# Kernel tuning notes

Measured on AMD Instinct MI355X. Metric: run time of the kernel, lower is better.

The kernel has to match this reference:

```python
import jax, jax.numpy as jnp
import numpy as np
import math

D_MODEL = 1024
NUM_HEADS = 16
HEAD_DIM = D_MODEL // NUM_HEADS
GAMMA = 1.0
B, T = 2, 2048
PHI_F = 8


def setup_inputs() -> dict:
    key = jax.random.key(0)
    ks = jax.random.split(key, 16)
    s = 0.02
    return {
        "query": jax.random.normal(ks[0], (B, T, D_MODEL), jnp.float32),
        "key": jax.random.normal(ks[1], (B, T, D_MODEL), jnp.float32),
        "value": jax.random.normal(ks[2], (B, T, D_MODEL), jnp.float32),
        "phi": jax.random.uniform(ks[3], (B, T, PHI_F), jnp.float32),
        "logvar": jax.random.normal(ks[4], (B, T, PHI_F), jnp.float32),
        "Wq": jax.random.normal(ks[5], (D_MODEL, D_MODEL), jnp.float32) * s,
        "bq": jnp.zeros((D_MODEL,), jnp.float32),
        "Wk": jax.random.normal(ks[6], (D_MODEL, D_MODEL), jnp.float32) * s,
        "bk": jnp.zeros((D_MODEL,), jnp.float32),
        "Wv": jax.random.normal(ks[7], (D_MODEL, D_MODEL), jnp.float32) * s,
        "bv": jnp.zeros((D_MODEL,), jnp.float32),
        "Wo": jax.random.normal(ks[8], (D_MODEL, D_MODEL), jnp.float32) * s,
        "bo": jnp.zeros((D_MODEL,), jnp.float32),
        "w_sigma": jnp.float32(1.0),
        "w_phi": jnp.float32(1.0),
    }


def reference(query, key, value, phi, logvar, Wq, bq, Wk, bk, Wv, bv, Wo, bo, w_sigma, w_phi):
    Bsz, Tq, _ = query.shape
    # projections (torch Linear: x @ W.T + b), split into heads -> (B, H, T, hd)
    def proj(x, W, b):
        return (x @ W.T + b).reshape(Bsz, Tq, NUM_HEADS, HEAD_DIM).transpose(0, 2, 1, 3)
    q = proj(query, Wq, bq)
    k = proj(key, Wk, bk)
    v = proj(value, Wv, bv)
    # raw scores (B, H, Tq, Tk)
    scores = jnp.einsum("bhqd,bhkd->bhqk", q, k) / math.sqrt(HEAD_DIM)
    # per-query token scalar biases: mean over feature dim -> (B, 1, T, 1)
    lv = logvar.mean(axis=-1)[:, None, :, None]
    ph = phi.mean(axis=-1)[:, None, :, None]
    scores = scores - w_sigma * lv
    scores = (scores - w_phi * (1.0 - ph)) / jnp.maximum(ph ** GAMMA, 1e-6)
    attn = jax.nn.softmax(scores, axis=-1)
    out = jnp.einsum("bhqk,bhkd->bhqd", attn, v)
    out = out.transpose(0, 2, 1, 3).reshape(Bsz, Tq, D_MODEL)
    return out @ Wo.T + bo
```

## Files before the change

### kernel.cpp

```cpp
#include <hip/hip_runtime.h>


typedef __bf16 bf16x8 __attribute__((ext_vector_type(8)));
typedef float f32x4 __attribute__((ext_vector_type(4)));
typedef unsigned short u16;
typedef unsigned int u32;
typedef u16 u16x8 __attribute__((ext_vector_type(8)));

#define GLD_TO_LDS(g, l) __builtin_amdgcn_global_load_lds( \
    (const __attribute__((address_space(1))) void*)(g),    \
    (__attribute__((address_space(3))) void*)(l), 16, 0, 0)

__device__ __forceinline__ u16 f2b(float f) {
  u32 u = __builtin_bit_cast(u32, f);
  u += 0x7fffu + ((u >> 16) & 1u);
  return (u16)(u >> 16);
}

__global__ __launch_bounds__(256) void prep_kernel(
    const float* __restrict__ query, const float* __restrict__ key,
    const float* __restrict__ value, const float* __restrict__ Wq,
    const float* __restrict__ Wk, const float* __restrict__ Wv,
    const float* __restrict__ Wo, const float* __restrict__ phi,
    u16* __restrict__ Xq, u16* __restrict__ Xk, u16* __restrict__ Xv,
    u16* __restrict__ Wqb, u16* __restrict__ Wkb, u16* __restrict__ Wvb,
    u16* __restrict__ Wob, float* __restrict__ rscale)
{
  const long gid = (long)blockIdx.x * 256 + threadIdx.x;
  const long e = gid * 4;
  const float* src; u16* dst; long off;
  if (e < 4194304L)       { src = query; dst = Xq;  off = e; }
  else if (e < 8388608L)  { src = key;   dst = Xk;  off = e - 4194304L; }
  else if (e < 12582912L) { src = value; dst = Xv;  off = e - 8388608L; }
  else if (e < 13631488L) { src = Wq;    dst = Wqb; off = e - 12582912L; }
  else if (e < 14680064L) { src = Wk;    dst = Wkb; off = e - 13631488L; }
  else if (e < 15728640L) { src = Wv;    dst = Wvb; off = e - 14680064L; }
  else                    { src = Wo;    dst = Wob; off = e - 15728640L; }
  const float4 v = *(const float4*)(src + off);
  ushort4 o;
  o.x = f2b(v.x); o.y = f2b(v.y); o.z = f2b(v.z); o.w = f2b(v.w);
  *(ushort4*)(dst + off) = o;

  if (gid < 4096) {
    const float4 p0 = *(const float4*)(phi + gid * 8);
    const float4 p1 = *(const float4*)(phi + gid * 8 + 4);
    const float mean = (p0.x + p0.y + p0.z + p0.w + p1.x + p1.y + p1.z + p1.w) * 0.125f;
    rscale[gid] = 1.4426950408889634f / (8.0f * fmaxf(mean, 1e-6f));
  }
}

template<int MODE>
__device__ __forceinline__ void gemm_body(
    u16* As, u16* Bs,
    const u16* __restrict__ A, const u16* __restrict__ Bw,
    const float* __restrict__ bias, void* __restrict__ Cout)
{
  constexpr int K = 1024;
  const int t = threadIdx.x;
  const int lane = t & 63, w = t >> 6;
  const int g = lane >> 4, c = lane & 15;
  const int m0 = blockIdx.y * 128, n0 = blockIdx.x * 128;
  const int srow = t >> 2, skc = (t & 3) * 8;
  const u16* gA = A + (size_t)(m0 + srow) * K + skc;
  const u16* gB = Bw + (size_t)(n0 + srow) * K + skc;
  u16* ldsA = As + w * 512;
  u16* ldsB = Bs + w * 512;
  const int wm = (w >> 1) * 64, wn = (w & 1) * 64;

  f32x4 acc[4][4] = {};

  for (int k0 = 0; k0 < K; k0 += 32) {
    GLD_TO_LDS(gA + k0, ldsA);
    GLD_TO_LDS(gA + 64 * K + k0, ldsA + 2048);
    GLD_TO_LDS(gB + k0, ldsB);
    GLD_TO_LDS(gB + 64 * K + k0, ldsB + 2048);
    __syncthreads();
    bf16x8 af[4], bfr[4];
#pragma unroll
    for (int mi = 0; mi < 4; ++mi)
      af[mi] = *(const bf16x8*)(As + (wm + mi * 16 + c) * 32 + g * 8);
#pragma unroll
    for (int ni = 0; ni < 4; ++ni)
      bfr[ni] = *(const bf16x8*)(Bs + (wn + ni * 16 + c) * 32 + g * 8);
#pragma unroll
    for (int mi = 0; mi < 4; ++mi)
#pragma unroll
      for (int ni = 0; ni < 4; ++ni)
        acc[mi][ni] = __builtin_amdgcn_mfma_f32_16x16x32_bf16(
            af[mi], bfr[ni], acc[mi][ni], 0, 0, 0);
    __syncthreads();
  }

#pragma unroll
  for (int ni = 0; ni < 4; ++ni) {
    const int ncol = n0 + wn + ni * 16 + c;
    const float bv = bias[ncol];
#pragma unroll
    for (int mi = 0; mi < 4; ++mi) {
#pragma unroll
      for (int r = 0; r < 4; ++r) {
        const int mrow = m0 + wm + mi * 16 + g * 4 + r;
        const float val = acc[mi][ni][r] + bv;
        if (MODE == 0) {
          const int bb = mrow >> 11, tt = mrow & 2047;
          const int hh = ncol >> 6, dd = ncol & 63;
          ((u16*)Cout)[((((size_t)bb * 16 + hh) * 2048 + tt) << 6) + dd] = f2b(val);
        } else {
          ((float*)Cout)[(size_t)mrow * 1024 + ncol] = val;
        }
      }
    }
  }
}

__global__ __launch_bounds__(256) void gemm_qkv_kernel(
    const u16* __restrict__ Xq, const u16* __restrict__ Xk, const u16* __restrict__ Xv,
    const u16* __restrict__ Wqb, const u16* __restrict__ Wkb, const u16* __restrict__ Wvb,
    const float* __restrict__ bq, const float* __restrict__ bk, const float* __restrict__ bv,
    u16* __restrict__ Qh, u16* __restrict__ Kh, u16* __restrict__ Vh)
{
  __shared__ __align__(16) u16 As[4096], Bs[4096];
  const int z = blockIdx.z;
  const u16* A = (z == 0) ? Xq : (z == 1) ? Xk : Xv;
  const u16* W = (z == 0) ? Wqb : (z == 1) ? Wkb : Wvb;
  const float* bias = (z == 0) ? bq : (z == 1) ? bk : bv;
  u16* C = (z == 0) ? Qh : (z == 1) ? Kh : Vh;
  gemm_body<0>(As, Bs, A, W, bias, C);
}

__global__ __launch_bounds__(256) void gemm_o_kernel(
    const u16* __restrict__ Oh, const u16* __restrict__ Wob,
    const float* __restrict__ bo, float* __restrict__ out)
{
  __shared__ __align__(16) u16 As[4096], Bs[4096];
  gemm_body<1>(As, Bs, Oh, Wob, bo, out);
}

__global__ __launch_bounds__(256) void transpose_v_kernel(
    const u16* __restrict__ Vh, u16* __restrict__ Vt)
{
  __shared__ __align__(16) u16 tile[64][72];
  const int bh = blockIdx.y, t0 = blockIdx.x * 64;
  const int tid = threadIdx.x;
  const int r = tid >> 3, cc = (tid & 7) * 8;
  const u16* src = Vh + ((size_t)bh * 2048 + t0) * 64;
#pragma unroll
  for (int it = 0; it < 2; ++it)
    *(u16x8*)&tile[r + 32 * it][cc] = *(const u16x8*)(src + (size_t)(r + 32 * it) * 64 + cc);
  __syncthreads();
  u16* dst = Vt + (size_t)bh * 64 * 2048 + t0;
#pragma unroll
  for (int it = 0; it < 2; ++it) {
    const int d = r + 32 * it;
    u16x8 v;
#pragma unroll
    for (int j = 0; j < 8; ++j) v[j] = tile[cc + j][d];
    *(u16x8*)(dst + (size_t)d * 2048 + cc) = v;
  }
}

__global__ __launch_bounds__(256) void attn_kernel(
    const u16* __restrict__ Qh, const u16* __restrict__ Kh,
    const u16* __restrict__ Vt, const float* __restrict__ rscale,
    u16* __restrict__ Oh)
{
  __shared__ __align__(16) u16 Ks[2][4096];
  __shared__ __align__(16) u16 Vs[2][4096];
  __shared__ __align__(16) u16 Pl[4][1024];

  const u32 orig = blockIdx.y * 32 + blockIdx.x;
  const u32 newL = (orig & 7u) * 128u + (orig >> 3);
  const int qx = newL & 31, bh = newL >> 5;
  const int b = bh >> 4, h = bh & 15;

  const int t = threadIdx.x;
  const int w = t >> 6, lane = t & 63;
  const int g = lane >> 4, c = lane & 15;
  const int q0 = qx * 64 + w * 16;
  const int swz = (c & 7) << 4;

  const u16* Qb = Qh + (size_t)bh * (2048 * 64);
  const u16* Kb = Kh + (size_t)bh * (2048 * 64);
  const u16* Vb = Vt + (size_t)bh * (64 * 2048);

  const int sr = t >> 3;
  const int sx = ((t & 7) ^ (sr & 7)) * 8;

  const float rs = rscale[b * 2048 + q0 + c];
  bf16x8 qf0, qf1;
  {
    const u16x8 a0 = *(const u16x8*)(Qb + (size_t)(q0 + c) * 64 + g * 8);
    const u16x8 a1 = *(const u16x8*)(Qb + (size_t)(q0 + c) * 64 + 32 + g * 8);
    u16x8 o0, o1;
#pragma unroll
    for (int j = 0; j < 8; ++j) {
      o0[j] = f2b(__builtin_bit_cast(float, (u32)a0[j] << 16) * rs);
      o1[j] = f2b(__builtin_bit_cast(float, (u32)a1[j] << 16) * rs);
    }
    qf0 = __builtin_bit_cast(bf16x8, o0);
    qf1 = __builtin_bit_cast(bf16x8, o1);
  }

  float m[4], l[4];
#pragma unroll
  for (int r = 0; r < 4; ++r) { m[r] = -3.0e38f; l[r] = 0.0f; }
  f32x4 acc[4] = {};
  u16* const Pw = &Pl[w][0];

#define STAGE(buf_, kc_) do {                                         \
    const u16* kg0 = Kb + (size_t)((kc_) + sr) * 64 + sx;             \
    const u16* kg1 = Kb + (size_t)((kc_) + 32 + sr) * 64 + sx;        \
    const u16* vg0 = Vb + (size_t)sr * 2048 + (kc_) + sx;             \
    const u16* vg1 = Vb + (size_t)(32 + sr) * 2048 + (kc_) + sx;      \
    u16* kd = &Ks[buf_][w * 512];                                     \
    u16* vd = &Vs[buf_][w * 512];                                     \
    GLD_TO_LDS(kg0, kd);                                              \
    GLD_TO_LDS(kg1, kd + 2048);                                       \
    GLD_TO_LDS(vg0, vd);                                              \
    GLD_TO_LDS(vg1, vd + 2048);                                       \
  } while (0)

  STAGE(0, 0);

  for (int kc = 0; kc < 2048; kc += 64) {
    const int buf = (kc >> 6) & 1;
    if (kc + 64 < 2048) {
      STAGE(buf ^ 1, kc + 64);
      asm volatile("s_waitcnt vmcnt(4)" ::: "memory");
    } else {
      asm volatile("s_waitcnt vmcnt(0)" ::: "memory");
    }
    __builtin_amdgcn_s_barrier();

    const u16* Kt = &Ks[buf][0];
    const u16* Vq = &Vs[buf][0];

    f32x4 s[4];
#pragma unroll
    for (int j = 0; j < 4; ++j) {
      const int rk = j * 16 + c;
      const bf16x8 k0 = *(const bf16x8*)(Kt + rk * 64 + ((((g << 4)) ^ swz) >> 1));
      const bf16x8 k1 = *(const bf16x8*)(Kt + rk * 64 + (((64 | (g << 4)) ^ swz) >> 1));
      const f32x4 z = {};
      s[j] = __builtin_amdgcn_mfma_f32_16x16x32_bf16(qf0, k0, z, 0, 0, 0);
      s[j] = __builtin_amdgcn_mfma_f32_16x16x32_bf16(qf1, k1, s[j], 0, 0, 0);
    }

    bf16x8 vf[4][2];
#pragma unroll
    for (int dt = 0; dt < 4; ++dt) {
      const int rv = dt * 16 + c;
#pragma unroll
      for (int kk = 0; kk < 2; ++kk)
        vf[dt][kk] = *(const bf16x8*)(Vq + rv * 64 + ((((kk << 6) | (g << 4)) ^ swz) >> 1));
    }

    float tl[4];
    bool need = false;
#pragma unroll
    for (int r = 0; r < 4; ++r) {
      tl[r] = fmaxf(fmaxf(s[0][r], s[1][r]), fmaxf(s[2][r], s[3][r]));
      need |= (tl[r] > m[r] + 8.0f);
    }
    if (__any(need)) {
#pragma unroll
      for (int d = 1; d < 16; d <<= 1)
#pragma unroll
        for (int r = 0; r < 4; ++r)
          tl[r] = fmaxf(tl[r], __shfl_xor(tl[r], d));
#pragma unroll
      for (int r = 0; r < 4; ++r) {
        const float mn = fmaxf(m[r], tl[r]);
        const float corr = __builtin_amdgcn_exp2f(m[r] - mn);
        m[r] = mn;
        l[r] *= corr;
#pragma unroll
        for (int dt = 0; dt < 4; ++dt) acc[dt][r] *= corr;
      }
    }

#pragma unroll
    for (int j = 0; j < 4; ++j)
#pragma unroll
      for (int r = 0; r < 4; ++r) {
        const float p = __builtin_amdgcn_exp2f(s[j][r] - m[r]);
        l[r] += p;
        const int prow = g * 4 + r;
        Pw[prow * 64 + ((((j * 16 + c) * 2) ^ ((prow & 7) << 4)) >> 1)] = f2b(p);
      }
    const bf16x8 pA0 = *(const bf16x8*)(Pw + c * 64 + (((0 | (g << 4)) ^ swz) >> 1));
    const bf16x8 pA1 = *(const bf16x8*)(Pw + c * 64 + (((64 | (g << 4)) ^ swz) >> 1));
#pragma unroll
    for (int dt = 0; dt < 4; ++dt) {
      acc[dt] = __builtin_amdgcn_mfma_f32_16x16x32_bf16(pA0, vf[dt][0], acc[dt], 0, 0, 0);
      acc[dt] = __builtin_amdgcn_mfma_f32_16x16x32_bf16(pA1, vf[dt][1], acc[dt], 0, 0, 0);
    }

    __builtin_amdgcn_s_barrier();
  }
#undef STAGE

#pragma unroll
  for (int d = 1; d < 16; d <<= 1)
#pragma unroll
    for (int r = 0; r < 4; ++r)
      l[r] += __shfl_xor(l[r], d);

  float inv[4];
#pragma unroll
  for (int r = 0; r < 4; ++r) inv[r] = 1.0f / l[r];
#pragma unroll
  for (int dt = 0; dt < 4; ++dt)
#pragma unroll
    for (int r = 0; r < 4; ++r) {
      const int trow = q0 + g * 4 + r;
      const int dd = dt * 16 + c;
      Oh[(((size_t)b * 2048 + trow) * 16 + h) * 64 + dd] = f2b(acc[dt][r] * inv[r]);
    }
}

extern "C" void kernel_launch(void* const* d_in, const int* in_sizes, int n_in,
                              void* d_out, int out_size, void* d_ws, size_t ws_size,
                              hipStream_t stream) {
  const float* query = (const float*)d_in[0];
  const float* key_  = (const float*)d_in[1];
  const float* value = (const float*)d_in[2];
  const float* phi   = (const float*)d_in[3];
  const float* Wq = (const float*)d_in[5];
  const float* bq = (const float*)d_in[6];
  const float* Wk = (const float*)d_in[7];
  const float* bk = (const float*)d_in[8];
  const float* Wv = (const float*)d_in[9];
  const float* bv = (const float*)d_in[10];
  const float* Wo = (const float*)d_in[11];
  const float* bo = (const float*)d_in[12];

  char* ws = (char*)d_ws;
  const size_t MB = 1u << 20;
  u16* Xq  = (u16*)(ws);
  u16* Xk  = (u16*)(ws + 8 * MB);
  u16* Xv  = (u16*)(ws + 16 * MB);
  u16* Wqb = (u16*)(ws + 24 * MB);
  u16* Wkb = (u16*)(ws + 26 * MB);
  u16* Wvb = (u16*)(ws + 28 * MB);
  u16* Wob = (u16*)(ws + 30 * MB);
  u16* Qh  = (u16*)(ws + 32 * MB);
  u16* Kh  = (u16*)(ws + 40 * MB);
  u16* Vh  = (u16*)(ws + 48 * MB);
  float* rscale = (float*)(ws + 56 * MB);
  u16* Oh = Xq;
  u16* Vt = Xk;

  prep_kernel<<<16384, 256, 0, stream>>>(query, key_, value, Wq, Wk, Wv, Wo, phi,
                                         Xq, Xk, Xv, Wqb, Wkb, Wvb, Wob, rscale);
  gemm_qkv_kernel<<<dim3(8, 32, 3), 256, 0, stream>>>(Xq, Xk, Xv, Wqb, Wkb, Wvb,
                                                      bq, bk, bv, Qh, Kh, Vh);
  transpose_v_kernel<<<dim3(32, 32), 256, 0, stream>>>(Vh, Vt);
  attn_kernel<<<dim3(32, 32), 256, 0, stream>>>(Qh, Kh, Vt, rscale, Oh);
  gemm_o_kernel<<<dim3(8, 32), 256, 0, stream>>>(Oh, Wob, bo, (float*)d_out);
}
```

Baseline: 288.0 us.

## Transpose attention MFMAs to keep P in registers; double-buffer GEMMs with swizzled grid

The attention kernel now computes S^T (K as A operand, Q as B), so each lane holds a single query column. The probabilities can then be packed straight into bf16 MFMA operands with no LDS round-trip for P. The row max and sum collapse to one scalar per lane, cutting the shuffles, and V fragments are gathered with 4-element LDS reads. The projection GEMMs gain double-buffered LDS staging with vmcnt waits, plus a block-index remap intended to improve L2 reuse. The costs are doubled GEMM LDS use and more V-load instructions.

```diff
diff --git a/kernel.cpp b/kernel.cpp
--- a/kernel.cpp
+++ b/kernel.cpp
@@ -2,6 +2,7 @@
 
 
 typedef __bf16 bf16x8 __attribute__((ext_vector_type(8)));
+typedef __bf16 bf16x4 __attribute__((ext_vector_type(4)));
 typedef float f32x4 __attribute__((ext_vector_type(4)));
 typedef unsigned short u16;
 typedef unsigned int u32;
@@ -51,7 +52,7 @@
 
 template<int MODE>
 __device__ __forceinline__ void gemm_body(
-    u16* As, u16* Bs,
+    u16 (*As)[4096], u16 (*Bs)[4096], int m0, int n0,
     const u16* __restrict__ A, const u16* __restrict__ Bw,
     const float* __restrict__ bias, void* __restrict__ Cout)
 {
@@ -59,37 +60,46 @@
   const int t = threadIdx.x;
   const int lane = t & 63, w = t >> 6;
   const int g = lane >> 4, c = lane & 15;
-  const int m0 = blockIdx.y * 128, n0 = blockIdx.x * 128;
   const int srow = t >> 2, skc = (t & 3) * 8;
   const u16* gA = A + (size_t)(m0 + srow) * K + skc;
   const u16* gB = Bw + (size_t)(n0 + srow) * K + skc;
-  u16* ldsA = As + w * 512;
-  u16* ldsB = Bs + w * 512;
   const int wm = (w >> 1) * 64, wn = (w & 1) * 64;
 
   f32x4 acc[4][4] = {};
 
-  for (int k0 = 0; k0 < K; k0 += 32) {
-    GLD_TO_LDS(gA + k0, ldsA);
-    GLD_TO_LDS(gA + 64 * K + k0, ldsA + 2048);
-    GLD_TO_LDS(gB + k0, ldsB);
-    GLD_TO_LDS(gB + 64 * K + k0, ldsB + 2048);
-    __syncthreads();
+#define STG(b_, k0_) do {                              \
+    GLD_TO_LDS(gA + (k0_), &As[b_][w * 512]);          \
+    GLD_TO_LDS(gA + 64 * K + (k0_), &As[b_][w * 512 + 2048]); \
+    GLD_TO_LDS(gB + (k0_), &Bs[b_][w * 512]);          \
+    GLD_TO_LDS(gB + 64 * K + (k0_), &Bs[b_][w * 512 + 2048]); \
+  } while (0)
+
+  STG(0, 0);
+  for (int i = 0; i < 32; ++i) {
+    const int buf = i & 1;
+    if (i < 31) {
+      STG(buf ^ 1, (i + 1) * 32);
+      asm volatile("s_waitcnt vmcnt(4)" ::: "memory");
+    } else {
+      asm volatile("s_waitcnt vmcnt(0)" ::: "memory");
+    }
+    __builtin_amdgcn_s_barrier();
     bf16x8 af[4], bfr[4];
 #pragma unroll
     for (int mi = 0; mi < 4; ++mi)
-      af[mi] = *(const bf16x8*)(As + (wm + mi * 16 + c) * 32 + g * 8);
+      af[mi] = *(const bf16x8*)(&As[buf][0] + (wm + mi * 16 + c) * 32 + g * 8);
 #pragma unroll
     for (int ni = 0; ni < 4; ++ni)
-      bfr[ni] = *(const bf16x8*)(Bs + (wn + ni * 16 + c) * 32 + g * 8);
+      bfr[ni] = *(const bf16x8*)(&Bs[buf][0] + (wn + ni * 16 + c) * 32 + g * 8);
 #pragma unroll
     for (int mi = 0; mi < 4; ++mi)
 #pragma unroll
       for (int ni = 0; ni < 4; ++ni)
         acc[mi][ni] = __builtin_amdgcn_mfma_f32_16x16x32_bf16(
             af[mi], bfr[ni], acc[mi][ni], 0, 0, 0);
-    __syncthreads();
-  }
+    __builtin_amdgcn_s_barrier();
+  }
+#undef STG
 
 #pragma unroll
   for (int ni = 0; ni < 4; ++ni) {
@@ -119,21 +129,25 @@
     const float* __restrict__ bq, const float* __restrict__ bk, const float* __restrict__ bv,
     u16* __restrict__ Qh, u16* __restrict__ Kh, u16* __restrict__ Vh)
 {
-  __shared__ __align__(16) u16 As[4096], Bs[4096];
-  const int z = blockIdx.z;
-  const u16* A = (z == 0) ? Xq : (z == 1) ? Xk : Xv;
-  const u16* W = (z == 0) ? Wqb : (z == 1) ? Wkb : Wvb;
-  const float* bias = (z == 0) ? bq : (z == 1) ? bk : bv;
-  u16* C = (z == 0) ? Qh : (z == 1) ? Kh : Vh;
-  gemm_body<0>(As, Bs, A, W, bias, C);
+  __shared__ __align__(16) u16 As[2][4096], Bs[2][4096];
+  const u32 n = blockIdx.z * 256u + blockIdx.y * 8u + blockIdx.x;
+  const u32 nl = (n & 7u) * 96u + (n >> 3);
+  const int bx = nl & 7, by = (nl >> 3) & 31, bz = nl >> 8;
+  const u16* A = (bz == 0) ? Xq : (bz == 1) ? Xk : Xv;
+  const u16* W = (bz == 0) ? Wqb : (bz == 1) ? Wkb : Wvb;
+  const float* bias = (bz == 0) ? bq : (bz == 1) ? bk : bv;
+  u16* C = (bz == 0) ? Qh : (bz == 1) ? Kh : Vh;
+  gemm_body<0>(As, Bs, by * 128, bx * 128, A, W, bias, C);
 }
 
 __global__ __launch_bounds__(256) void gemm_o_kernel(
     const u16* __restrict__ Oh, const u16* __restrict__ Wob,
     const float* __restrict__ bo, float* __restrict__ out)
 {
-  __shared__ __align__(16) u16 As[4096], Bs[4096];
-  gemm_body<1>(As, Bs, Oh, Wob, bo, out);
+  __shared__ __align__(16) u16 As[2][4096], Bs[2][4096];
+  const u32 n = blockIdx.y * 8u + blockIdx.x;
+  const u32 nl = (n & 7u) * 32u + (n >> 3);
+  gemm_body<1>(As, Bs, (int)(nl >> 3) * 128, (int)(nl & 7) * 128, Oh, Wob, bo, out);
 }
 
 __global__ __launch_bounds__(256) void transpose_v_kernel(
@@ -166,7 +180,6 @@
 {
   __shared__ __align__(16) u16 Ks[2][4096];
   __shared__ __align__(16) u16 Vs[2][4096];
-  __shared__ __align__(16) u16 Pl[4][1024];
 
   const u32 orig = blockIdx.y * 32 + blockIdx.x;
   const u32 newL = (orig & 7u) * 128u + (orig >> 3);
@@ -201,11 +214,8 @@
     qf1 = __builtin_bit_cast(bf16x8, o1);
   }
 
-  float m[4], l[4];
-#pragma unroll
-  for (int r = 0; r < 4; ++r) { m[r] = -3.0e38f; l[r] = 0.0f; }
+  float m = -3.0e38f, l = 0.0f;
   f32x4 acc[4] = {};
-  u16* const Pw = &Pl[w][0];
 
 #define STAGE(buf_, kc_) do {                                         \
     const u16* kg0 = Kb + (size_t)((kc_) + sr) * 64 + sx;             \
@@ -242,80 +252,77 @@
       const bf16x8 k0 = *(const bf16x8*)(Kt + rk * 64 + ((((g << 4)) ^ swz) >> 1));
       const bf16x8 k1 = *(const bf16x8*)(Kt + rk * 64 + (((64 | (g << 4)) ^ swz) >> 1));
       const f32x4 z = {};
-      s[j] = __builtin_amdgcn_mfma_f32_16x16x32_bf16(qf0, k0, z, 0, 0, 0);
-      s[j] = __builtin_amdgcn_mfma_f32_16x16x32_bf16(qf1, k1, s[j], 0, 0, 0);
-    }
-
-    bf16x8 vf[4][2];
+      s[j] = __builtin_amdgcn_mfma_f32_16x16x32_bf16(k0, qf0, z, 0, 0, 0);
+      s[j] = __builtin_amdgcn_mfma_f32_16x16x32_bf16(k1, qf1, s[j], 0, 0, 0);
+    }
+
+    float tl = s[0][0];
+#pragma unroll
+    for (int j = 0; j < 4; ++j)
+#pragma unroll
+      for (int r = 0; r < 4; ++r) tl = fmaxf(tl, s[j][r]);
+    if (__any(tl > m + 8.0f)) {
+      tl = fmaxf(tl, __shfl_xor(tl, 16));
+      tl = fmaxf(tl, __shfl_xor(tl, 32));
+      const float mn = fmaxf(m, tl);
+      const float corr = __builtin_amdgcn_exp2f(m - mn);
+      m = mn;
+      l *= corr;
+#pragma unroll
+      for (int dt = 0; dt < 4; ++dt)
+#pragma unroll
+        for (int r = 0; r < 4; ++r) acc[dt][r] *= corr;
+    }
+
+    float p[4][4];
+#pragma unroll
+    for (int j = 0; j < 4; ++j)
+#pragma unroll
+      for (int r = 0; r < 4; ++r) {
+        p[j][r] = __builtin_amdgcn_exp2f(s[j][r] - m);
+        l += p[j][r];
+      }
+    bf16x8 pb0, pb1;
+#pragma unroll
+    for (int jj = 0; jj < 8; ++jj) {
+      pb0[jj] = (__bf16)p[jj >> 2][jj & 3];
+      pb1[jj] = (__bf16)p[2 + (jj >> 2)][jj & 3];
+    }
+
 #pragma unroll
     for (int dt = 0; dt < 4; ++dt) {
       const int rv = dt * 16 + c;
-#pragma unroll
-      for (int kk = 0; kk < 2; ++kk)
-        vf[dt][kk] = *(const bf16x8*)(Vq + rv * 64 + ((((kk << 6) | (g << 4)) ^ swz) >> 1));
-    }
-
-    float tl[4];
-    bool need = false;
+      const u16* vrow = Vq + rv * 64;
+      const int xr = (rv & 7) << 4;
+      bf16x8 va0, va1;
+      const bf16x4 a0 = *(const bf16x4*)(vrow + (((g * 8) ^ xr) >> 1));
+      const bf16x4 a1 = *(const bf16x4*)(vrow + (((32 + g * 8) ^ xr) >> 1));
+      const bf16x4 a2 = *(const bf16x4*)(vrow + (((64 + g * 8) ^ xr) >> 1));
+      const bf16x4 a3 = *(const bf16x4*)(vrow + (((96 + g * 8) ^ xr) >> 1));
+#pragma unroll
+      for (int j = 0; j < 4; ++j) {
+        va0[j] = a0[j]; va0[4 + j] = a1[j];
+        va1[j] = a2[j]; va1[4 + j] = a3[j];
+      }
+      acc[dt] = __builtin_amdgcn_mfma_f32_16x16x32_bf16(va0, pb0, acc[dt], 0, 0, 0);
+      acc[dt] = __builtin_amdgcn_mfma_f32_16x16x32_bf16(va1, pb1, acc[dt], 0, 0, 0);
+    }
+
+    __builtin_amdgcn_s_barrier();
+  }
+#undef STAGE
+
+  l += __shfl_xor(l, 16);
+  l += __shfl_xor(l, 32);
+  const float inv = 1.0f / l;
+
+#pragma unroll
+  for (int dt = 0; dt < 4; ++dt)
 #pragma unroll
     for (int r = 0; r < 4; ++r) {
-      tl[r] = fmaxf(fmaxf(s[0][r], s[1][r]), fmaxf(s[2][r], s[3][r]));
-      need |= (tl[r] > m[r] + 8.0f);
-    }
-    if (__any(need)) {
-#pragma unroll
-      for (int d = 1; d < 16; d <<= 1)
-#pragma unroll
-        for (int r = 0; r < 4; ++r)
-          tl[r] = fmaxf(tl[r], __shfl_xor(tl[r], d));
-#pragma unroll
-      for (int r = 0; r < 4; ++r) {
-        const float mn = fmaxf(m[r], tl[r]);
-        const float corr = __builtin_amdgcn_exp2f(m[r] - mn);
-        m[r] = mn;
-        l[r] *= corr;
-#pragma unroll
-        for (int dt = 0; dt < 4; ++dt) acc[dt][r] *= corr;
-      }
-    }
-
-#pragma unroll
-    for (int j = 0; j < 4; ++j)
-#pragma unroll
-      for (int r = 0; r < 4; ++r) {
-        const float p = __builtin_amdgcn_exp2f(s[j][r] - m[r]);
-        l[r] += p;
-        const int prow = g * 4 + r;
-        Pw[prow * 64 + ((((j * 16 + c) * 2) ^ ((prow & 7) << 4)) >> 1)] = f2b(p);
-      }
-    const bf16x8 pA0 = *(const bf16x8*)(Pw + c * 64 + (((0 | (g << 4)) ^ swz) >> 1));
-    const bf16x8 pA1 = *(const bf16x8*)(Pw + c * 64 + (((64 | (g << 4)) ^ swz) >> 1));
-#pragma unroll
-    for (int dt = 0; dt < 4; ++dt) {
-      acc[dt] = __builtin_amdgcn_mfma_f32_16x16x32_bf16(pA0, vf[dt][0], acc[dt], 0, 0, 0);
-      acc[dt] = __builtin_amdgcn_mfma_f32_16x16x32_bf16(pA1, vf[dt][1], acc[dt], 0, 0, 0);
-    }
-
-    __builtin_amdgcn_s_barrier();
-  }
-#undef STAGE
-
-#pragma unroll
-  for (int d = 1; d < 16; d <<= 1)
-#pragma unroll
-    for (int r = 0; r < 4; ++r)
-      l[r] += __shfl_xor(l[r], d);
-
-  float inv[4];
-#pragma unroll
-  for (int r = 0; r < 4; ++r) inv[r] = 1.0f / l[r];
-#pragma unroll
-  for (int dt = 0; dt < 4; ++dt)
-#pragma unroll
-    for (int r = 0; r < 4; ++r) {
-      const int trow = q0 + g * 4 + r;
-      const int dd = dt * 16 + c;
-      Oh[(((size_t)b * 2048 + trow) * 16 + h) * 64 + dd] = f2b(acc[dt][r] * inv[r]);
+      const int trow = q0 + c;
+      const int dd = dt * 16 + g * 4 + r;
+      Oh[(((size_t)b * 2048 + trow) * 16 + h) * 64 + dd] = f2b(acc[dt][r] * inv);
     }
 }
 
```

New measurement: 258.4 us. -10.3%, faster.
